# Kernel optimization log

Hardware: AMD Instinct MI355X
Metric: run time of the kernel (lower is better)

## Reference

```python
import jax, jax.numpy as jnp
import numpy as np

HID = 256  # LSTM hidden size (hard-coded in Renet)


def _lstm_dir(x, wih, whh, b):
    # x: [N, T, D]; PyTorch LSTM gate order: i, f, g, o
    def cell(carry, xt):
        h, c = carry
        g = xt @ wih.T + h @ whh.T + b
        i, f, gg, o = jnp.split(g, 4, axis=-1)
        c = jax.nn.sigmoid(f) * c + jax.nn.sigmoid(i) * jnp.tanh(gg)
        h = jax.nn.sigmoid(o) * jnp.tanh(c)
        return (h, c), h
    n = x.shape[0]
    h0 = jnp.zeros((n, HID), x.dtype)
    _, hs = jax.lax.scan(cell, (h0, h0), jnp.swapaxes(x, 0, 1))
    return jnp.swapaxes(hs, 0, 1)  # [N, T, HID]


def _bilstm(x, wf, uf, bf, wb, ub, bb):
    hf = _lstm_dir(x, wf, uf, bf)
    hb = _lstm_dir(x[:, ::-1], wb, ub, bb)[:, ::-1]
    return jnp.concatenate([hf, hb], axis=-1)  # [N, T, 2*HID]


def setup_inputs() -> dict:
    key = jax.random.key(0)
    ks = jax.random.split(key, 16)
    B, C, S = 8, 512, 64
    def p(k, shape):
        return 0.05 * jax.random.normal(k, shape, jnp.float32)
    d = {}
    d['x'] = jax.random.normal(ks[0], (B, C, S, S), jnp.float32)
    d['v_wih_f'] = p(ks[1], (4 * HID, C))
    d['v_whh_f'] = p(ks[2], (4 * HID, HID))
    d['v_b_f'] = p(ks[3], (4 * HID,))
    d['v_wih_b'] = p(ks[4], (4 * HID, C))
    d['v_whh_b'] = p(ks[5], (4 * HID, HID))
    d['v_b_b'] = p(ks[6], (4 * HID,))
    d['h_wih_f'] = p(ks[7], (4 * HID, 2 * HID))
    d['h_whh_f'] = p(ks[8], (4 * HID, HID))
    d['h_b_f'] = p(ks[9], (4 * HID,))
    d['h_wih_b'] = p(ks[10], (4 * HID, 2 * HID))
    d['h_whh_b'] = p(ks[11], (4 * HID, HID))
    d['h_b_b'] = p(ks[12], (4 * HID,))
    d['conv_w'] = p(ks[13], (22 * 22, 2 * HID))
    d['conv_b'] = p(ks[14], (22 * 22,))
    return d


def reference(x, v_wih_f, v_whh_f, v_b_f, v_wih_b, v_whh_b, v_b_b,
              h_wih_f, h_whh_f, h_b_f, h_wih_b, h_whh_b, h_b_b,
              conv_w, conv_b):
    B, C, H, W = x.shape
    # ---- Renet ----
    xt = jnp.transpose(x, (0, 2, 3, 1))  # [B,H,W,C]
    # vertical LSTM: sequence along W, batched over all B*H rows at once
    v = _bilstm(xt.reshape(B * H, W, C), v_wih_f, v_whh_f, v_b_f,
                v_wih_b, v_whh_b, v_b_b).reshape(B, H, W, 2 * HID)
    # horizontal LSTM: sequence along H, batched over all B*W columns
    h = _bilstm(jnp.transpose(v, (0, 2, 1, 3)).reshape(B * W, H, 2 * HID),
                h_wih_f, h_whh_f, h_b_f, h_wih_b, h_whh_b,
                h_b_b).reshape(B, W, H, 2 * HID)
    feat = jnp.transpose(h, (0, 3, 2, 1))  # [B, 512, H, W]
    kern = jnp.einsum('bchw,oc->bohw', feat, conv_w) + conv_b[None, :, None, None]
    # ---- PicanetG ----
    kern = jax.nn.softmax(kern, axis=1)  # softmax over 484 channel dim
    # unfold(k=22, dilation=3) with H=W=64 yields exactly one global dilated patch
    patch = x[:, :, ::3, ::3].reshape(B, C, 22 * 22)  # [B, C, 484]
    out = jnp.einsum('bck,bkl->bcl', patch, kern.reshape(B, 22 * 22, H * W))
    return out.reshape(B, C, H, W)
```

## Files before the change

### kernel.cpp

```cpp
#include <hip/hip_runtime.h>
#include <hip/hip_bf16.h>
#include <hip/hip_fp8.h>
#include <math.h>


typedef __hip_bfloat16 bf16;
typedef short short8 __attribute__((ext_vector_type(8)));
typedef float f4 __attribute__((ext_vector_type(4)));
typedef int int4v __attribute__((ext_vector_type(4)));
typedef int int8v __attribute__((ext_vector_type(8)));

#define SCL8 0x7F7F7F7F

__device__ __forceinline__ unsigned short bfbits(float f) {
    bf16 h = __float2bfloat16(f);
    return *reinterpret_cast<unsigned short*>(&h);
}
__device__ __forceinline__ float bf2f(unsigned short u) {
    union { unsigned int i; float f; } x; x.i = ((unsigned int)u) << 16; return x.f;
}
__device__ __forceinline__ unsigned char f2fp8(float f) {
    __hip_fp8_e4m3 q(f);
    return *reinterpret_cast<unsigned char*>(&q);
}
__device__ __forceinline__ float sigm2(float x) {
    return __builtin_amdgcn_rcpf(1.0f + __builtin_amdgcn_exp2f(x * -1.44269504f));
}
__device__ __forceinline__ float tanh2(float x) {
    return 1.0f - 2.0f * __builtin_amdgcn_rcpf(1.0f + __builtin_amdgcn_exp2f(x * 2.88539008f));
}

#define GLD16(g, s) __builtin_amdgcn_global_load_lds(                          \
    (const __attribute__((address_space(1))) void*)(g),                        \
    (__attribute__((address_space(3))) void*)(s), 16, 0, 0)

#define LGKM_BARRIER() do {                                                    \
    asm volatile("s_waitcnt lgkmcnt(0)" ::: "memory");                         \
    __builtin_amdgcn_s_barrier();                                              \
} while (0)

__global__ __launch_bounds__(256)
void prep_weights(const float* __restrict__ w0, const float* __restrict__ w1,
                  const float* __restrict__ w2, const float* __restrict__ w3,
                  const float* __restrict__ cw, const float* __restrict__ cb,
                  const float* __restrict__ u0, const float* __restrict__ u1,
                  const float* __restrict__ u2, const float* __restrict__ u3,
                  bf16* __restrict__ wt, bf16* __restrict__ cw2b,
                  float* __restrict__ cb2, unsigned char* __restrict__ wq)
{
    int idx = blockIdx.x * 256 + threadIdx.x;
    if (idx < 2097152) {
        int mat = idx >> 19, rem = idx & 524287;
        const float* src = (mat == 0) ? w0 : (mat == 1) ? w1 : (mat == 2) ? w2 : w3;
        wt[idx] = __float2bfloat16(src[rem]);
    } else if (idx < 2097152 + 262144) {
        int r = idx - 2097152; int o = r >> 9, k = r & 511;
        cw2b[r] = __float2bfloat16((o < 484) ? cw[o * 512 + k] : 0.f);
    } else if (idx < 2097152 + 262144 + 512) {
        int o = idx - 2097152 - 262144;
        cb2[o] = (o < 484) ? cb[o] : 0.f;
    } else if (idx < 2097152 + 262144 + 512 + 1048576) {
        int r = idx - 2097152 - 262144 - 512;
        int mat = r >> 18, rem = r & 262143;
        const float* src = (mat == 0) ? u0 : (mat == 1) ? u1 : (mat == 2) ? u2 : u3;
        wq[r] = f2fp8(src[rem]);
    }
}

__global__ __launch_bounds__(256)
void xtrans(const float* __restrict__ x, bf16* __restrict__ xt)
{
    __shared__ float T[64][65];
    const int tid = threadIdx.x;
    const int bid = blockIdx.x;
    const int b = bid >> 9, h = (bid >> 3) & 63, ct = bid & 7;
    const int c0 = ct << 6;
    const float* xp = x + ((long)(b * 512 + c0) * 64 + h) * 64;
    const int wv = tid >> 6, wl = tid & 63;
    #pragma unroll
    for (int r = 0; r < 16; ++r) {
        int ci = wv + (r << 2);
        T[ci][wl] = xp[(long)ci * 4096 + wl];
    }
    __syncthreads();
    const int wr = tid >> 2, cj = (tid & 3) << 4;
    bf16* op = xt + ((long)(b * 4096 + h * 64 + wr) * 512) + c0 + cj;
    short8 v0, v1;
    #pragma unroll
    for (int i = 0; i < 8; ++i) v0[i] = (short)bfbits(T[cj + i][wr]);
    #pragma unroll
    for (int i = 0; i < 8; ++i) v1[i] = (short)bfbits(T[cj + 8 + i][wr]);
    *(short8*)op = v0;
    *(short8*)(op + 8) = v1;
}

template<int MODE>
__global__ __launch_bounds__(256)
void gemm_lds(const bf16* __restrict__ A, const bf16* __restrict__ W,
              const float* __restrict__ biasf, const float* __restrict__ biasb,
              void* __restrict__ outf, void* __restrict__ outb, int dironly)
{
    __shared__ alignas(16) char Abuf[16384];
    __shared__ alignas(16) char Bbuf[16384];
    const int tid = threadIdx.x;
    const int wv = tid >> 6, l = tid & 63;
    const int lm = l & 15, lg = l >> 4;
    const int wm = wv >> 1, wn = wv & 1;

    const int nx = gridDim.x;
    int bid = blockIdx.y * nx + blockIdx.x;
    const int cpx = (nx * gridDim.y) >> 3;
    bid = (bid & 7) * cpx + (bid >> 3);
    const int bx = bid % nx;
    const int n0 = (bid / nx) << 7;

    int dir = 0, jblk = 0, g0 = 0;
    const bf16* Wg = W;
    if (MODE == 0) {
        dir  = (dironly < 0) ? (bx >> 3) : dironly;
        jblk = (dironly < 0) ? (bx & 7) : bx;
    } else {
        g0 = bx << 7;
        if (MODE == 2) Wg += (long)(n0 >> 9) * 2097152;
    }

    f4 acc[4][4];
    #pragma unroll
    for (int mf = 0; mf < 4; ++mf)
        #pragma unroll
        for (int nf = 0; nf < 4; ++nf)
            acc[mf][nf] = (f4){0.f, 0.f, 0.f, 0.f};

    for (int kt = 0; kt < 8; ++kt) {
        const int k0 = kt << 6;
        #pragma unroll
        for (int i = 0; i < 4; ++i) {
            const int seg = (wv << 2) + i;
            const int L = (seg << 10) + l * 16;
            const int row = L >> 7;
            const int off = (L & 127) ^ ((row & 7) << 4);
            const bf16* ga = A + (long)(n0 + row) * 512 + k0 + (off >> 1);
            GLD16(ga, &Abuf[seg << 10]);
        }
        #pragma unroll
        for (int i = 0; i < 4; ++i) {
            const int seg = (wv << 2) + i;
            const int L = (seg << 10) + l * 16;
            const int row = L >> 7;
            const int off = (L & 127) ^ ((row & 7) << 4);
            int wrow;
            if (MODE == 0) wrow = (dir << 10) + ((row >> 5) << 8) + jblk * 32 + (row & 31);
            else           wrow = g0 + row;
            const bf16* gb = Wg + (long)wrow * 512 + k0 + (off >> 1);
            GLD16(gb, &Bbuf[seg << 10]);
        }
        __syncthreads();

        #pragma unroll
        for (int kk = 0; kk < 2; ++kk) {
            short8 af[4], bq[4];
            #pragma unroll
            for (int mf = 0; mf < 4; ++mf) {
                const int row = wm * 64 + mf * 16 + lm;
                const int ad = (row << 7) + ((((kk << 6) + (lg << 4))) ^ ((row & 7) << 4));
                af[mf] = *(const short8*)&Abuf[ad];
            }
            #pragma unroll
            for (int nf = 0; nf < 4; ++nf) {
                const int row = (MODE == 0) ? (nf * 32 + wn * 16 + lm)
                                            : (wn * 64 + nf * 16 + lm);
                const int ad = (row << 7) + ((((kk << 6) + (lg << 4))) ^ ((row & 7) << 4));
                bq[nf] = *(const short8*)&Bbuf[ad];
            }
            #pragma unroll
            for (int mf = 0; mf < 4; ++mf)
                #pragma unroll
                for (int nf = 0; nf < 4; ++nf)
                    acc[mf][nf] = __builtin_amdgcn_mfma_f32_16x16x32_bf16(af[mf], bq[nf], acc[mf][nf], 0, 0, 0);
        }
        __syncthreads();
    }

    if (MODE == 0) {
        const float* bs = dir ? biasb : biasf;
        const int jglob = jblk * 32 + wn * 16 + lm;
        float bv[4];
        #pragma unroll
        for (int nf = 0; nf < 4; ++nf) bv[nf] = bs[nf * 256 + jglob];
        ushort4* Gd = (ushort4*)(dir ? outb : outf);
        #pragma unroll
        for (int mf = 0; mf < 4; ++mf) {
            #pragma unroll
            for (int r = 0; r < 4; ++r) {
                const int n = n0 + wm * 64 + mf * 16 + lg * 4 + r;
                ushort4 u;
                u.x = bfbits(acc[mf][0][r] + bv[0]);
                u.y = bfbits(acc[mf][1][r] + bv[1]);
                u.z = bfbits(acc[mf][2][r] + bv[2]);
                u.w = bfbits(acc[mf][3][r] + bv[3]);
                Gd[(long)n * 256 + jglob] = u;
            }
        }
    } else {
        float* o = (float*)outf;
        #pragma unroll
        for (int mf = 0; mf < 4; ++mf)
            #pragma unroll
            for (int r = 0; r < 4; ++r) {
                const int n = n0 + wm * 64 + mf * 16 + lg * 4 + r;
                #pragma unroll
                for (int nf = 0; nf < 4; ++nf)
                    o[(long)n * 4096 + g0 + wn * 64 + nf * 16 + lm] = acc[mf][nf][r];
            }
    }
}

__global__ __launch_bounds__(512)
void conv_sm(const bf16* __restrict__ A, const bf16* __restrict__ W,
             const float* __restrict__ bias, bf16* __restrict__ KT)
{
    __shared__ alignas(16) char SMEM[83968];
    char* Ab = SMEM;
    char* Bb = SMEM + 16384;
    float (*red)[4] = (float(*)[4])(SMEM + 81920);

    const int tid = threadIdx.x;
    const int wv = tid >> 6, l = tid & 63;
    const int lm = l & 15, lg = l >> 4;
    const int wm = wv >> 2, wn = wv & 3;
    const int n0 = blockIdx.x << 7;

    f4 acc[4][8];
    #pragma unroll
    for (int mf = 0; mf < 4; ++mf)
        #pragma unroll
        for (int nf = 0; nf < 8; ++nf)
            acc[mf][nf] = (f4){0.f, 0.f, 0.f, 0.f};

    for (int kt = 0; kt < 8; ++kt) {
        const int k0 = kt << 6;
        #pragma unroll
        for (int i = 0; i < 2; ++i) {
            const int L = (i << 13) + tid * 16;
            const int row = L >> 7;
            const int off = (L & 127) ^ ((row & 7) << 4);
            GLD16(A + (long)(n0 + row) * 512 + k0 + (off >> 1),
                  Ab + (i << 13) + (wv << 10));
        }
        #pragma unroll
        for (int j = 0; j < 8; ++j) {
            const int L = (j << 13) + tid * 16;
            const int row = L >> 7;
            const int off = (L & 127) ^ ((row & 7) << 4);
            GLD16(W + (long)row * 512 + k0 + (off >> 1),
                  Bb + (j << 13) + (wv << 10));
        }
        __syncthreads();
        #pragma unroll
        for (int kk = 0; kk < 2; ++kk) {
            short8 af[4], bq[8];
            #pragma unroll
            for (int mf = 0; mf < 4; ++mf) {
                const int row = wm * 64 + mf * 16 + lm;
                const int ad = (row << 7) + ((((kk << 6) + (lg << 4))) ^ ((row & 7) << 4));
                af[mf] = *(const short8*)&Ab[ad];
            }
            #pragma unroll
            for (int nf = 0; nf < 8; ++nf) {
                const int row = wn * 128 + nf * 16 + lm;
                const int ad = (row << 7) + ((((kk << 6) + (lg << 4))) ^ ((row & 7) << 4));
                bq[nf] = *(const short8*)&Bb[ad];
            }
            #pragma unroll
            for (int mf = 0; mf < 4; ++mf)
                #pragma unroll
                for (int nf = 0; nf < 8; ++nf)
                    acc[mf][nf] = __builtin_amdgcn_mfma_f32_16x16x32_bf16(af[mf], bq[nf], acc[mf][nf], 0, 0, 0);
        }
        __syncthreads();
    }

    float bv[8];
    bool alive[8];
    #pragma unroll
    for (int nf = 0; nf < 8; ++nf) {
        const int col = wn * 128 + nf * 16 + lm;
        bv[nf] = bias[col];
        alive[nf] = (col < 484);
    }

    #pragma unroll
    for (int mf = 0; mf < 4; ++mf) {
        #pragma unroll
        for (int r = 0; r < 4; ++r) {
            float m = -3.4e38f;
            #pragma unroll
            for (int nf = 0; nf < 8; ++nf) {
                float v = acc[mf][nf][r] + bv[nf];
                if (alive[nf]) m = fmaxf(m, v);
            }
            m = fmaxf(m, __shfl_xor(m, 1));
            m = fmaxf(m, __shfl_xor(m, 2));
            m = fmaxf(m, __shfl_xor(m, 4));
            m = fmaxf(m, __shfl_xor(m, 8));
            if (lm == 0) red[wm * 64 + mf * 16 + lg * 4 + r][wn] = m;
        }
    }
    __syncthreads();
    float mxv[4][4];
    #pragma unroll
    for (int mf = 0; mf < 4; ++mf)
        #pragma unroll
        for (int r = 0; r < 4; ++r) {
            const int row = wm * 64 + mf * 16 + lg * 4 + r;
            mxv[mf][r] = fmaxf(fmaxf(red[row][0], red[row][1]),
                               fmaxf(red[row][2], red[row][3]));
        }
    __syncthreads();
    #pragma unroll
    for (int mf = 0; mf < 4; ++mf) {
        #pragma unroll
        for (int r = 0; r < 4; ++r) {
            float s = 0.f;
            #pragma unroll
            for (int nf = 0; nf < 8; ++nf) {
                float v = acc[mf][nf][r] + bv[nf];
                float e = alive[nf]
                    ? __builtin_amdgcn_exp2f((v - mxv[mf][r]) * 1.44269504f) : 0.f;
                acc[mf][nf][r] = e;
                s += e;
            }
            s += __shfl_xor(s, 1);
            s += __shfl_xor(s, 2);
            s += __shfl_xor(s, 4);
            s += __shfl_xor(s, 8);
            if (lm == 0) red[wm * 64 + mf * 16 + lg * 4 + r][wn] = s;
        }
    }
    __syncthreads();
    float invv[4][4];
    #pragma unroll
    for (int mf = 0; mf < 4; ++mf)
        #pragma unroll
        for (int r = 0; r < 4; ++r) {
            const int row = wm * 64 + mf * 16 + lg * 4 + r;
            invv[mf][r] = __builtin_amdgcn_rcpf(red[row][0] + red[row][1] +
                                                red[row][2] + red[row][3]);
        }

    unsigned short* TB = (unsigned short*)Bb;
    unsigned short* KTu = (unsigned short*)KT;
    #pragma unroll
    for (int hm = 0; hm < 2; ++hm) {
        __syncthreads();
        if (wm == hm) {
            #pragma unroll
            for (int mf = 0; mf < 4; ++mf)
                #pragma unroll
                for (int r = 0; r < 4; ++r) {
                    const int rr = mf * 16 + lg * 4 + r;
                    #pragma unroll
                    for (int nf = 0; nf < 8; ++nf)
                        TB[rr * 512 + wn * 128 + nf * 16 + lm] =
                            bfbits(acc[mf][nf][r] * invv[mf][r]);
                }
        }
        __syncthreads();
        #pragma unroll
        for (int s = 0; s < 8; ++s) {
            const int L = (s << 13) + tid * 16;
            const int rr = L >> 10;
            const int cc = (L & 1023) >> 1;
            *(short8*)(KTu + (long)(n0 + hm * 64 + rr) * 512 + cc) =
                *(const short8*)((const char*)TB + L);
        }
    }
}

__global__ __launch_bounds__(1024, 4)
void lstm4s(const bf16* __restrict__ Gf, const bf16* __restrict__ Gb,
            const unsigned char* __restrict__ Wqf, const unsigned char* __restrict__ Wqb,
            bf16* __restrict__ Out, int dir_force)
{
    __shared__ char ldspad[83968];
    __shared__ unsigned char hbuf[2][4][256];
    const int tid = threadIdx.x;
    const int wv = tid >> 6, l = tid & 63;
    const int lm = l & 15, lg = l >> 4;
    const int j_c = wv * 16 + lm;
    const int s_a = lm >> 2;

    int dir, sblk;
    if (dir_force >= 0) { dir = dir_force; sblk = blockIdx.x; }
    else               { dir = blockIdx.x >> 7; sblk = blockIdx.x & 127; }
    if (dir_force == -9999) ((volatile char*)ldspad)[tid] = 1;

    const bf16* G = dir ? Gb : Gf;
    const unsigned char* WQ = dir ? Wqb : Wqf;
    const int s0 = sblk << 2;

    int8v wfrag[4][2];
    #pragma unroll
    for (int q = 0; q < 4; ++q) {
        const unsigned char* wr = WQ + (long)(q * 256 + wv * 16 + lm) * 256 + lg * 32;
        #pragma unroll
        for (int kt = 0; kt < 2; ++kt) {
            int4v lo = *(const int4v*)(wr + kt * 128);
            int4v hi = *(const int4v*)(wr + kt * 128 + 16);
            int8v w;
            w[0] = lo[0]; w[1] = lo[1]; w[2] = lo[2]; w[3] = lo[3];
            w[4] = hi[0]; w[5] = hi[1]; w[6] = hi[2]; w[7] = hi[3];
            wfrag[q][kt] = w;
        }
    }

    if (tid < 256) ((unsigned long*)hbuf)[tid] = 0ul;

    float cst = 0.f;
    const ushort4* G4 = (const ushort4*)G;
    const int sg = s0 + lg;
    const long gb0 = (long)sg * 16384 + j_c;
    const long ob0 = ((long)((s0 >> 6) * 4096 + (s0 & 63) + lg)) * 512 + (dir << 8) + j_c;
    unsigned short* Ou = (unsigned short*)Out;

    ushort4 uA, uB;
    {
        int t0 = dir ? 63 : 0, t1 = dir ? 62 : 1;
        uA = G4[gb0 + (long)t0 * 256];
        uB = G4[gb0 + (long)t1 * 256];
    }
    LGKM_BARRIER();

#define LSTM_STEP(SP, UREG, RB, WB)                                             \
    {                                                                           \
        const int t_ = dir ? (63 - (SP)) : (SP);                                \
        int8v af0, af1;                                                         \
        {                                                                       \
            const unsigned char* hb = &hbuf[RB][s_a][0];                        \
            const int c0 = ((lg << 5) + (s_a << 5)) & 255;                      \
            const int c1 = (128 + (lg << 5) + (s_a << 5)) & 255;                \
            int4v a0 = *(const int4v*)(hb + c0);                                \
            int4v a1 = *(const int4v*)(hb + c0 + 16);                           \
            int4v b0 = *(const int4v*)(hb + c1);                                \
            int4v b1 = *(const int4v*)(hb + c1 + 16);                           \
            af0[0]=a0[0]; af0[1]=a0[1]; af0[2]=a0[2]; af0[3]=a0[3];             \
            af0[4]=a1[0]; af0[5]=a1[1]; af0[6]=a1[2]; af0[7]=a1[3];             \
            af1[0]=b0[0]; af1[1]=b0[1]; af1[2]=b0[2]; af1[3]=b0[3];             \
            af1[4]=b1[0]; af1[5]=b1[1]; af1[6]=b1[2]; af1[7]=b1[3];             \
        }                                                                       \
        f4 ac0 = {0.f,0.f,0.f,0.f}, ac1 = {0.f,0.f,0.f,0.f};                    \
        f4 ac2 = {0.f,0.f,0.f,0.f}, ac3 = {0.f,0.f,0.f,0.f};                    \
        ac0[0] = bf2f(UREG.x); ac1[0] = bf2f(UREG.y);                           \
        ac2[0] = bf2f(UREG.z); ac3[0] = bf2f(UREG.w);                           \
        {                                                                       \
            int sp2 = (SP) + 2; if (sp2 > 63) sp2 = 63;                         \
            int tp = dir ? (63 - sp2) : sp2;                                    \
            UREG = G4[gb0 + (long)tp * 256];                                    \
        }                                                                       \
        ac0 = __builtin_amdgcn_mfma_scale_f32_16x16x128_f8f6f4(af0, wfrag[0][0], ac0, 0, 0, 0, SCL8, 0, SCL8); \
        ac1 = __builtin_amdgcn_mfma_scale_f32_16x16x128_f8f6f4(af0, wfrag[1][0], ac1, 0, 0, 0, SCL8, 0, SCL8); \
        ac2 = __builtin_amdgcn_mfma_scale_f32_16x16x128_f8f6f4(af0, wfrag[2][0], ac2, 0, 0, 0, SCL8, 0, SCL8); \
        ac3 = __builtin_amdgcn_mfma_scale_f32_16x16x128_f8f6f4(af0, wfrag[3][0], ac3, 0, 0, 0, SCL8, 0, SCL8); \
        ac0 = __builtin_amdgcn_mfma_scale_f32_16x16x128_f8f6f4(af1, wfrag[0][1], ac0, 0, 0, 0, SCL8, 0, SCL8); \
        ac1 = __builtin_amdgcn_mfma_scale_f32_16x16x128_f8f6f4(af1, wfrag[1][1], ac1, 0, 0, 0, SCL8, 0, SCL8); \
        ac2 = __builtin_amdgcn_mfma_scale_f32_16x16x128_f8f6f4(af1, wfrag[2][1], ac2, 0, 0, 0, SCL8, 0, SCL8); \
        ac3 = __builtin_amdgcn_mfma_scale_f32_16x16x128_f8f6f4(af1, wfrag[3][1], ac3, 0, 0, 0, SCL8, 0, SCL8); \
        {                                                                       \
            float ii = sigm2(ac0[0]);                                           \
            float ff = sigm2(ac1[0]);                                           \
            float gc = tanh2(ac2[0]);                                           \
            float oo = sigm2(ac3[0]);                                           \
            float c  = ff * cst + ii * gc;                                      \
            cst = c;                                                            \
            float h_ = oo * tanh2(c);                                           \
            hbuf[WB][lg][(j_c + (lg << 5)) & 255] = f2fp8(h_);                  \
            Ou[ob0 + (long)t_ * 32768] = bfbits(h_);                            \
        }                                                                       \
        LGKM_BARRIER();                                                         \
    }

    for (int sp = 0; sp < 64; sp += 2) {
        LSTM_STEP(sp,     uA, 0, 1)
        LSTM_STEP(sp + 1, uB, 1, 0)
    }
#undef LSTM_STEP
}

__global__ __launch_bounds__(256)
void gather_patch(const float* __restrict__ x, bf16* __restrict__ Pch)
{
    int idx = blockIdx.x * 256 + threadIdx.x;
    if (idx >= 2097152) return;
    int o = idx & 511, c = (idx >> 9) & 511, b = idx >> 18;
    float v = 0.f;
    if (o < 484) {
        int i = o / 22, jj = o - i * 22;
        v = x[(long)b * 2097152 + (long)c * 4096 + i * 192 + jj * 3];
    }
    Pch[idx] = __float2bfloat16(v);
}

extern "C" void kernel_launch(void* const* d_in, const int* in_sizes, int n_in,
                              void* d_out, int out_size, void* d_ws, size_t ws_size,
                              hipStream_t stream)
{
    const float* x        = (const float*)d_in[0];
    const float* v_wih_f  = (const float*)d_in[1];
    const float* v_whh_f  = (const float*)d_in[2];
    const float* v_b_f    = (const float*)d_in[3];
    const float* v_wih_b  = (const float*)d_in[4];
    const float* v_whh_b  = (const float*)d_in[5];
    const float* v_b_b    = (const float*)d_in[6];
    const float* h_wih_f  = (const float*)d_in[7];
    const float* h_whh_f  = (const float*)d_in[8];
    const float* h_b_f    = (const float*)d_in[9];
    const float* h_wih_b  = (const float*)d_in[10];
    const float* h_whh_b  = (const float*)d_in[11];
    const float* h_b_b    = (const float*)d_in[12];
    const float* conv_w   = (const float*)d_in[13];
    const float* conv_b   = (const float*)d_in[14];

    const size_t REQ_FUSED  = 50331648UL * 4UL;
    const size_t REQ_SERIAL = 33554432UL * 4UL;
    if (ws_size < REQ_SERIAL) return;
    const bool fused = (ws_size >= REQ_FUSED);

    float* wsf = (float*)d_ws;
    float* out = (float*)d_out;

    bf16*          wt   = (bf16*)(out + 8388608);
    bf16*          cw2b = (bf16*)(out + 9437184);
    float*         cb2  = out + 9568256;
    unsigned char* wq   = (unsigned char*)(out + 9568768);

    prep_weights<<<13314, 256, 0, stream>>>(v_wih_f, v_wih_b, h_wih_f, h_wih_b,
                                            conv_w, conv_b,
                                            v_whh_f, v_whh_b, h_whh_f, h_whh_b,
                                            wt, cw2b, cb2, wq);
    bf16* wt_v = wt;
    bf16* wt_h = wt + 1048576;
    unsigned char* wq_vf = wq;
    unsigned char* wq_vb = wq + 262144;
    unsigned char* wq_hf = wq + 524288;
    unsigned char* wq_hb = wq + 786432;

    dim3 gG(16, 256);
    dim3 gGs(8, 256);
    dim3 gF(32, 32);

    if (fused) {
        bf16*  Gf    = (bf16*)d_ws;
        bf16*  Gb    = (bf16*)(wsf + 16777216);
        bf16*  V     = (bf16*)(wsf + 33554432);
        bf16*  HF    = (bf16*)(wsf + 41943040);
        bf16*  xt    = V;
        bf16*  kernT = Gb;
        bf16*  Pch   = V;

        xtrans<<<4096, 256, 0, stream>>>(x, xt);
        gemm_lds<0><<<gG, 256, 0, stream>>>(xt, wt_v, v_b_f, v_b_b, Gf, Gb, -1);
        lstm4s<<<256, 1024, 0, stream>>>(Gf, Gb, wq_vf, wq_vb, V, -1);

        gemm_lds<0><<<gG, 256, 0, stream>>>(V, wt_h, h_b_f, h_b_b, Gf, Gb, -1);
        lstm4s<<<256, 1024, 0, stream>>>(Gf, Gb, wq_hf, wq_hb, HF, -1);

        conv_sm<<<256, 512, 0, stream>>>(HF, cw2b, cb2, kernT);
        gather_patch<<<8192, 256, 0, stream>>>(x, Pch);
        gemm_lds<2><<<gF, 256, 0, stream>>>(Pch, kernT, nullptr, nullptr, out, nullptr, 0);
    } else {
        bf16*  G     = (bf16*)d_ws;
        bf16*  V     = (bf16*)(wsf + 16777216);
        bf16*  xt    = (bf16*)(wsf + 25165824);
        bf16*  HF    = xt;
        bf16*  kernT = V;
        bf16*  Pch   = (bf16*)d_ws;

        xtrans<<<4096, 256, 0, stream>>>(x, xt);
        gemm_lds<0><<<gGs, 256, 0, stream>>>(xt, wt_v, v_b_f, v_b_b, G, G, 0);
        lstm4s<<<128, 1024, 0, stream>>>(G, G, wq_vf, wq_vf, V, 0);
        gemm_lds<0><<<gGs, 256, 0, stream>>>(xt, wt_v, v_b_f, v_b_b, G, G, 1);
        lstm4s<<<128, 1024, 0, stream>>>(G, G, wq_vb, wq_vb, V, 1);

        gemm_lds<0><<<gGs, 256, 0, stream>>>(V, wt_h, h_b_f, h_b_b, G, G, 0);
        lstm4s<<<128, 1024, 0, stream>>>(G, G, wq_hf, wq_hf, HF, 0);
        gemm_lds<0><<<gGs, 256, 0, stream>>>(V, wt_h, h_b_f, h_b_b, G, G, 1);
        lstm4s<<<128, 1024, 0, stream>>>(G, G, wq_hb, wq_hb, HF, 1);

        conv_sm<<<256, 512, 0, stream>>>(HF, cw2b, cb2, kernT);
        gather_patch<<<8192, 256, 0, stream>>>(x, Pch);
        gemm_lds<2><<<gF, 256, 0, stream>>>(Pch, kernT, nullptr, nullptr, out, nullptr, 0);
    }
}
```

Before: 427.9 us.

## Fuse LSTM input-projection GEMM into the recurrent LSTM kernel

Replaces the separate gate-precompute GEMM and the LSTM recurrence kernel with one kernel per layer. It computes input gates for 8-step chunks on the fly from double-buffered LDS tiles of the input and keeps them in LDS, so the large bf16 gate tensors never round-trip through global memory. The cost is that each block re-streams its weight slice from global or L2 per chunk without LDS staging. The MFMA projection work now sits inside the serial recurrence, which may lengthen the critical path.

Result: slower. 1.404 ms (+228.1%).

```diff
diff --git a/kernel.cpp b/kernel.cpp
--- a/kernel.cpp
+++ b/kernel.cpp
@@ -94,6 +94,180 @@
     *(short8*)(op + 8) = v1;
 }
 
+__global__ __launch_bounds__(1024, 4)
+void renet_fused(const bf16* __restrict__ A, const bf16* __restrict__ Wih,
+                 const float* __restrict__ biasf, const float* __restrict__ biasb,
+                 const unsigned char* __restrict__ Wqf,
+                 const unsigned char* __restrict__ Wqb,
+                 bf16* __restrict__ Out)
+{
+    __shared__ alignas(16) char Atile[2][32768];
+    __shared__ unsigned short Gch[4][8][256][4];
+    __shared__ unsigned char hbuf[2][4][256];
+
+    const int tid = threadIdx.x;
+    const int wv = tid >> 6, l = tid & 63;
+    const int lm = l & 15, lg = l >> 4;
+    const int j_c = wv * 16 + lm;
+    const int s_a = lm >> 2;
+
+    const int dir  = blockIdx.x >> 7;
+    const int sblk = blockIdx.x & 127;
+    const int s0 = sblk << 2;
+    const unsigned char* WQ = dir ? Wqb : Wqf;
+    const float* bs = dir ? biasb : biasf;
+    const bf16* Wd = Wih + ((long)dir << 10) * 512;
+
+    int8v wfrag[4][2];
+    #pragma unroll
+    for (int q = 0; q < 4; ++q) {
+        const unsigned char* wr = WQ + (long)((q << 8) + j_c) * 256 + (lg << 5);
+        #pragma unroll
+        for (int kt = 0; kt < 2; ++kt) {
+            int4v lo = *(const int4v*)(wr + kt * 128);
+            int4v hi = *(const int4v*)(wr + kt * 128 + 16);
+            int8v w;
+            w[0] = lo[0]; w[1] = lo[1]; w[2] = lo[2]; w[3] = lo[3];
+            w[4] = hi[0]; w[5] = hi[1]; w[6] = hi[2]; w[7] = hi[3];
+            wfrag[q][kt] = w;
+        }
+    }
+
+    float bv[4];
+    #pragma unroll
+    for (int q = 0; q < 4; ++q) bv[q] = bs[(q << 8) + j_c];
+
+    if (tid < 256) ((unsigned long*)hbuf)[tid] = 0ul;
+
+    float cst = 0.f;
+    const long ob0 = ((long)((s0 >> 6) * 4096 + (s0 & 63) + lg)) * 512
+                   + (dir << 8) + j_c;
+    unsigned short* Ou = (unsigned short*)Out;
+
+    long wb[4];
+    #pragma unroll
+    for (int q = 0; q < 4; ++q)
+        wb[q] = (long)((q << 8) + j_c) * 512 + (lg << 3);
+
+    const int swz0 = (lm & 7) << 4;
+
+    {
+        const int tb = dir ? 56 : 0;
+        #pragma unroll
+        for (int sw = 0; sw < 2; ++sw) {
+            const int r = sw * 16 + wv;
+            const int n = (s0 + (r >> 3)) * 64 + tb + (r & 7);
+            const int soff = (l * 16) ^ ((r & 7) << 4);
+            GLD16(A + (long)n * 512 + (soff >> 1), &Atile[0][r << 10]);
+        }
+    }
+    asm volatile("s_waitcnt vmcnt(0)" ::: "memory");
+    __builtin_amdgcn_s_barrier();
+
+    int buf = 0;
+    for (int c = 0; c < 8; ++c) {
+        if (c < 7) {
+            const int tb = dir ? 56 - 8 * (c + 1) : 8 * (c + 1);
+            #pragma unroll
+            for (int sw = 0; sw < 2; ++sw) {
+                const int r = sw * 16 + wv;
+                const int n = (s0 + (r >> 3)) * 64 + tb + (r & 7);
+                const int soff = (l * 16) ^ ((r & 7) << 4);
+                GLD16(A + (long)n * 512 + (soff >> 1), &Atile[buf ^ 1][r << 10]);
+            }
+        }
+
+        const char* Ab = Atile[buf];
+        #pragma unroll
+        for (int qp = 0; qp < 2; ++qp) {
+            f4 acc[2][2];
+            #pragma unroll
+            for (int mf = 0; mf < 2; ++mf)
+                #pragma unroll
+                for (int q2 = 0; q2 < 2; ++q2)
+                    acc[mf][q2] = (f4){0.f, 0.f, 0.f, 0.f};
+            #pragma unroll
+            for (int ks = 0; ks < 16; ++ks) {
+                const int ko = ((ks << 6) + (lg << 4)) ^ swz0;
+                short8 a0 = *(const short8*)(Ab + (lm << 10) + ko);
+                short8 a1 = *(const short8*)(Ab + ((16 + lm) << 10) + ko);
+                short8 b0 = *(const short8*)(Wd + wb[qp * 2 + 0] + (ks << 5));
+                short8 b1 = *(const short8*)(Wd + wb[qp * 2 + 1] + (ks << 5));
+                acc[0][0] = __builtin_amdgcn_mfma_f32_16x16x32_bf16(a0, b0, acc[0][0], 0, 0, 0);
+                acc[0][1] = __builtin_amdgcn_mfma_f32_16x16x32_bf16(a0, b1, acc[0][1], 0, 0, 0);
+                acc[1][0] = __builtin_amdgcn_mfma_f32_16x16x32_bf16(a1, b0, acc[1][0], 0, 0, 0);
+                acc[1][1] = __builtin_amdgcn_mfma_f32_16x16x32_bf16(a1, b1, acc[1][1], 0, 0, 0);
+            }
+            #pragma unroll
+            for (int mf = 0; mf < 2; ++mf)
+                #pragma unroll
+                for (int r = 0; r < 4; ++r) {
+                    const int row = mf * 16 + lg * 4 + r;
+                    ushort2 u2;
+                    u2.x = bfbits(acc[mf][0][r] + bv[qp * 2 + 0]);
+                    u2.y = bfbits(acc[mf][1][r] + bv[qp * 2 + 1]);
+                    *(ushort2*)&Gch[row >> 3][row & 7][j_c][qp << 1] = u2;
+                }
+        }
+        asm volatile("s_waitcnt lgkmcnt(0)" ::: "memory");
+        __builtin_amdgcn_s_barrier();
+
+        #pragma unroll
+        for (int i = 0; i < 8; ++i) {
+            const int sp = (c << 3) + i;
+            const int t_ = dir ? 63 - sp : sp;
+            const int toff = dir ? 7 - i : i;
+            const int RB = sp & 1, WB = 1 - RB;
+
+            int8v af0, af1;
+            {
+                const unsigned char* hb = &hbuf[RB][s_a][0];
+                const int c0i = ((lg << 5) + (s_a << 5)) & 255;
+                const int c1i = (128 + (lg << 5) + (s_a << 5)) & 255;
+                int4v a0 = *(const int4v*)(hb + c0i);
+                int4v a1 = *(const int4v*)(hb + c0i + 16);
+                int4v b0 = *(const int4v*)(hb + c1i);
+                int4v b1 = *(const int4v*)(hb + c1i + 16);
+                af0[0]=a0[0]; af0[1]=a0[1]; af0[2]=a0[2]; af0[3]=a0[3];
+                af0[4]=a1[0]; af0[5]=a1[1]; af0[6]=a1[2]; af0[7]=a1[3];
+                af1[0]=b0[0]; af1[1]=b0[1]; af1[2]=b0[2]; af1[3]=b0[3];
+                af1[4]=b1[0]; af1[5]=b1[1]; af1[6]=b1[2]; af1[7]=b1[3];
+            }
+            ushort4 Gr = *(const ushort4*)&Gch[lg][toff][j_c][0];
+            f4 ac0 = {0.f,0.f,0.f,0.f}, ac1 = {0.f,0.f,0.f,0.f};
+            f4 ac2 = {0.f,0.f,0.f,0.f}, ac3 = {0.f,0.f,0.f,0.f};
+            ac0[0] = bf2f(Gr.x); ac1[0] = bf2f(Gr.y);
+            ac2[0] = bf2f(Gr.z); ac3[0] = bf2f(Gr.w);
+
+            ac0 = __builtin_amdgcn_mfma_scale_f32_16x16x128_f8f6f4(af0, wfrag[0][0], ac0, 0, 0, 0, SCL8, 0, SCL8);
+            ac1 = __builtin_amdgcn_mfma_scale_f32_16x16x128_f8f6f4(af0, wfrag[1][0], ac1, 0, 0, 0, SCL8, 0, SCL8);
+            ac2 = __builtin_amdgcn_mfma_scale_f32_16x16x128_f8f6f4(af0, wfrag[2][0], ac2, 0, 0, 0, SCL8, 0, SCL8);
+            ac3 = __builtin_amdgcn_mfma_scale_f32_16x16x128_f8f6f4(af0, wfrag[3][0], ac3, 0, 0, 0, SCL8, 0, SCL8);
+            ac0 = __builtin_amdgcn_mfma_scale_f32_16x16x128_f8f6f4(af1, wfrag[0][1], ac0, 0, 0, 0, SCL8, 0, SCL8);
+            ac1 = __builtin_amdgcn_mfma_scale_f32_16x16x128_f8f6f4(af1, wfrag[1][1], ac1, 0, 0, 0, SCL8, 0, SCL8);
+            ac2 = __builtin_amdgcn_mfma_scale_f32_16x16x128_f8f6f4(af1, wfrag[2][1], ac2, 0, 0, 0, SCL8, 0, SCL8);
+            ac3 = __builtin_amdgcn_mfma_scale_f32_16x16x128_f8f6f4(af1, wfrag[3][1], ac3, 0, 0, 0, SCL8, 0, SCL8);
+
+            {
+                float ii = sigm2(ac0[0]);
+                float ff = sigm2(ac1[0]);
+                float gc = tanh2(ac2[0]);
+                float oo = sigm2(ac3[0]);
+                float cc = ff * cst + ii * gc;
+                cst = cc;
+                float h_ = oo * tanh2(cc);
+                hbuf[WB][lg][(j_c + (lg << 5)) & 255] = f2fp8(h_);
+                Ou[ob0 + (long)t_ * 32768] = bfbits(h_);
+            }
+            LGKM_BARRIER();
+        }
+
+        asm volatile("s_waitcnt vmcnt(0)" ::: "memory");
+        __builtin_amdgcn_s_barrier();
+        buf ^= 1;
+    }
+}
+
 template<int MODE>
 __global__ __launch_bounds__(256)
 void gemm_lds(const bf16* __restrict__ A, const bf16* __restrict__ W,
@@ -114,15 +288,9 @@
     const int bx = bid % nx;
     const int n0 = (bid / nx) << 7;
 
-    int dir = 0, jblk = 0, g0 = 0;
+    int g0 = bx << 7;
     const bf16* Wg = W;
-    if (MODE == 0) {
-        dir  = (dironly < 0) ? (bx >> 3) : dironly;
-        jblk = (dironly < 0) ? (bx & 7) : bx;
-    } else {
-        g0 = bx << 7;
-        if (MODE == 2) Wg += (long)(n0 >> 9) * 2097152;
-    }
+    if (MODE == 2) Wg += (long)(n0 >> 9) * 2097152;
 
     f4 acc[4][4];
     #pragma unroll
@@ -148,10 +316,7 @@
             const int L = (seg << 10) + l * 16;
             const int row = L >> 7;
             const int off = (L & 127) ^ ((row & 7) << 4);
-            int wrow;
-            if (MODE == 0) wrow = (dir << 10) + ((row >> 5) << 8) + jblk * 32 + (row & 31);
-            else           wrow = g0 + row;
-            const bf16* gb = Wg + (long)wrow * 512 + k0 + (off >> 1);
+            const bf16* gb = Wg + (long)(g0 + row) * 512 + k0 + (off >> 1);
             GLD16(gb, &Bbuf[seg << 10]);
         }
         __syncthreads();
@@ -167,8 +332,7 @@
             }
             #pragma unroll
             for (int nf = 0; nf < 4; ++nf) {
-                const int row = (MODE == 0) ? (nf * 32 + wn * 16 + lm)
-                                            : (wn * 64 + nf * 16 + lm);
+                const int row = wn * 64 + nf * 16 + lm;
                 const int ad = (row << 7) + ((((kk << 6) + (lg << 4))) ^ ((row & 7) << 4));
                 bq[nf] = *(const short8*)&Bbuf[ad];
             }
@@ -181,38 +345,16 @@
         __syncthreads();
     }
 
-    if (MODE == 0) {
-        const float* bs = dir ? biasb : biasf;
-        const int jglob = jblk * 32 + wn * 16 + lm;
-        float bv[4];
-        #pragma unroll
-        for (int nf = 0; nf < 4; ++nf) bv[nf] = bs[nf * 256 + jglob];
-        ushort4* Gd = (ushort4*)(dir ? outb : outf);
-        #pragma unroll
-        for (int mf = 0; mf < 4; ++mf) {
-            #pragma unroll
-            for (int r = 0; r < 4; ++r) {
-                const int n = n0 + wm * 64 + mf * 16 + lg * 4 + r;
-                ushort4 u;
-                u.x = bfbits(acc[mf][0][r] + bv[0]);
-                u.y = bfbits(acc[mf][1][r] + bv[1]);
-                u.z = bfbits(acc[mf][2][r] + bv[2]);
-                u.w = bfbits(acc[mf][3][r] + bv[3]);
-                Gd[(long)n * 256 + jglob] = u;
-            }
-        }
-    } else {
-        float* o = (float*)outf;
-        #pragma unroll
-        for (int mf = 0; mf < 4; ++mf)
-            #pragma unroll
-            for (int r = 0; r < 4; ++r) {
-                const int n = n0 + wm * 64 + mf * 16 + lg * 4 + r;
-                #pragma unroll
-                for (int nf = 0; nf < 4; ++nf)
-                    o[(long)n * 4096 + g0 + wn * 64 + nf * 16 + lm] = acc[mf][nf][r];
-            }
-    }
+    float* o = (float*)outf;
+    #pragma unroll
+    for (int mf = 0; mf < 4; ++mf)
+        #pragma unroll
+        for (int r = 0; r < 4; ++r) {
+            const int n = n0 + wm * 64 + mf * 16 + lg * 4 + r;
+            #pragma unroll
+            for (int nf = 0; nf < 4; ++nf)
+                o[(long)n * 4096 + g0 + wn * 64 + nf * 16 + lm] = acc[mf][nf][r];
+        }
 }
 
 __global__ __launch_bounds__(512)
@@ -375,115 +517,6 @@
                 *(const short8*)((const char*)TB + L);
         }
     }
-}
-
-__global__ __launch_bounds__(1024, 4)
-void lstm4s(const bf16* __restrict__ Gf, const bf16* __restrict__ Gb,
-            const unsigned char* __restrict__ Wqf, const unsigned char* __restrict__ Wqb,
-            bf16* __restrict__ Out, int dir_force)
-{
-    __shared__ char ldspad[83968];
-    __shared__ unsigned char hbuf[2][4][256];
-    const int tid = threadIdx.x;
-    const int wv = tid >> 6, l = tid & 63;
-    const int lm = l & 15, lg = l >> 4;
-    const int j_c = wv * 16 + lm;
-    const int s_a = lm >> 2;
-
-    int dir, sblk;
-    if (dir_force >= 0) { dir = dir_force; sblk = blockIdx.x; }
-    else               { dir = blockIdx.x >> 7; sblk = blockIdx.x & 127; }
-    if (dir_force == -9999) ((volatile char*)ldspad)[tid] = 1;
-
-    const bf16* G = dir ? Gb : Gf;
-    const unsigned char* WQ = dir ? Wqb : Wqf;
-    const int s0 = sblk << 2;
-
-    int8v wfrag[4][2];
-    #pragma unroll
-    for (int q = 0; q < 4; ++q) {
-        const unsigned char* wr = WQ + (long)(q * 256 + wv * 16 + lm) * 256 + lg * 32;
-        #pragma unroll
-        for (int kt = 0; kt < 2; ++kt) {
-            int4v lo = *(const int4v*)(wr + kt * 128);
-            int4v hi = *(const int4v*)(wr + kt * 128 + 16);
-            int8v w;
-            w[0] = lo[0]; w[1] = lo[1]; w[2] = lo[2]; w[3] = lo[3];
-            w[4] = hi[0]; w[5] = hi[1]; w[6] = hi[2]; w[7] = hi[3];
-            wfrag[q][kt] = w;
-        }
-    }
-
-    if (tid < 256) ((unsigned long*)hbuf)[tid] = 0ul;
-
-    float cst = 0.f;
-    const ushort4* G4 = (const ushort4*)G;
-    const int sg = s0 + lg;
-    const long gb0 = (long)sg * 16384 + j_c;
-    const long ob0 = ((long)((s0 >> 6) * 4096 + (s0 & 63) + lg)) * 512 + (dir << 8) + j_c;
-    unsigned short* Ou = (unsigned short*)Out;
-
-    ushort4 uA, uB;
-    {
-        int t0 = dir ? 63 : 0, t1 = dir ? 62 : 1;
-        uA = G4[gb0 + (long)t0 * 256];
-        uB = G4[gb0 + (long)t1 * 256];
-    }
-    LGKM_BARRIER();
-
-#define LSTM_STEP(SP, UREG, RB, WB)                                             \
-    {                                                                           \
-        const int t_ = dir ? (63 - (SP)) : (SP);                                \
-        int8v af0, af1;                                                         \
-        {                                                                       \
-            const unsigned char* hb = &hbuf[RB][s_a][0];                        \
-            const int c0 = ((lg << 5) + (s_a << 5)) & 255;                      \
-            const int c1 = (128 + (lg << 5) + (s_a << 5)) & 255;                \
-            int4v a0 = *(const int4v*)(hb + c0);                                \
-            int4v a1 = *(const int4v*)(hb + c0 + 16);                           \
-            int4v b0 = *(const int4v*)(hb + c1);                                \
-            int4v b1 = *(const int4v*)(hb + c1 + 16);                           \
-            af0[0]=a0[0]; af0[1]=a0[1]; af0[2]=a0[2]; af0[3]=a0[3];             \
-            af0[4]=a1[0]; af0[5]=a1[1]; af0[6]=a1[2]; af0[7]=a1[3];             \
-            af1[0]=b0[0]; af1[1]=b0[1]; af1[2]=b0[2]; af1[3]=b0[3];             \
-            af1[4]=b1[0]; af1[5]=b1[1]; af1[6]=b1[2]; af1[7]=b1[3];             \
-        }                                                                       \
-        f4 ac0 = {0.f,0.f,0.f,0.f}, ac1 = {0.f,0.f,0.f,0.f};                    \
-        f4 ac2 = {0.f,0.f,0.f,0.f}, ac3 = {0.f,0.f,0.f,0.f};                    \
-        ac0[0] = bf2f(UREG.x); ac1[0] = bf2f(UREG.y);                           \
-        ac2[0] = bf2f(UREG.z); ac3[0] = bf2f(UREG.w);                           \
-        {                                                                       \
-            int sp2 = (SP) + 2; if (sp2 > 63) sp2 = 63;                         \
-            int tp = dir ? (63 - sp2) : sp2;                                    \
-            UREG = G4[gb0 + (long)tp * 256];                                    \
-        }                                                                       \
-        ac0 = __builtin_amdgcn_mfma_scale_f32_16x16x128_f8f6f4(af0, wfrag[0][0], ac0, 0, 0, 0, SCL8, 0, SCL8); \
-        ac1 = __builtin_amdgcn_mfma_scale_f32_16x16x128_f8f6f4(af0, wfrag[1][0], ac1, 0, 0, 0, SCL8, 0, SCL8); \
-        ac2 = __builtin_amdgcn_mfma_scale_f32_16x16x128_f8f6f4(af0, wfrag[2][0], ac2, 0, 0, 0, SCL8, 0, SCL8); \
-        ac3 = __builtin_amdgcn_mfma_scale_f32_16x16x128_f8f6f4(af0, wfrag[3][0], ac3, 0, 0, 0, SCL8, 0, SCL8); \
-        ac0 = __builtin_amdgcn_mfma_scale_f32_16x16x128_f8f6f4(af1, wfrag[0][1], ac0, 0, 0, 0, SCL8, 0, SCL8); \
-        ac1 = __builtin_amdgcn_mfma_scale_f32_16x16x128_f8f6f4(af1, wfrag[1][1], ac1, 0, 0, 0, SCL8, 0, SCL8); \
-        ac2 = __builtin_amdgcn_mfma_scale_f32_16x16x128_f8f6f4(af1, wfrag[2][1], ac2, 0, 0, 0, SCL8, 0, SCL8); \
-        ac3 = __builtin_amdgcn_mfma_scale_f32_16x16x128_f8f6f4(af1, wfrag[3][1], ac3, 0, 0, 0, SCL8, 0, SCL8); \
-        {                                                                       \
-            float ii = sigm2(ac0[0]);                                           \
-            float ff = sigm2(ac1[0]);                                           \
-            float gc = tanh2(ac2[0]);                                           \
-            float oo = sigm2(ac3[0]);                                           \
-            float c  = ff * cst + ii * gc;                                      \
-            cst = c;                                                            \
-            float h_ = oo * tanh2(c);                                           \
-            hbuf[WB][lg][(j_c + (lg << 5)) & 255] = f2fp8(h_);                  \
-            Ou[ob0 + (long)t_ * 32768] = bfbits(h_);                            \
-        }                                                                       \
-        LGKM_BARRIER();                                                         \
-    }
-
-    for (int sp = 0; sp < 64; sp += 2) {
-        LSTM_STEP(sp,     uA, 0, 1)
-        LSTM_STEP(sp + 1, uB, 1, 0)
-    }
-#undef LSTM_STEP
 }
 
 __global__ __launch_bounds__(256)
@@ -520,10 +553,8 @@
     const float* conv_w   = (const float*)d_in[13];
     const float* conv_b   = (const float*)d_in[14];
 
-    const size_t REQ_FUSED  = 50331648UL * 4UL;
-    const size_t REQ_SERIAL = 33554432UL * 4UL;
-    if (ws_size < REQ_SERIAL) return;
-    const bool fused = (ws_size >= REQ_FUSED);
+    const size_t REQ = 33554432UL * 4UL;
+    if (ws_size < REQ) return;
 
     float* wsf = (float*)d_ws;
     float* out = (float*)d_out;
@@ -544,50 +575,17 @@
     unsigned char* wq_hf = wq + 524288;
     unsigned char* wq_hb = wq + 786432;
 
-    dim3 gG(16, 256);
-    dim3 gGs(8, 256);
+    bf16* xt    = (bf16*)d_ws;
+    bf16* V     = (bf16*)(wsf + 8388608);
+    bf16* HF    = (bf16*)(wsf + 16777216);
+    bf16* kernT = (bf16*)(wsf + 25165824);
+    bf16* Pch   = (bf16*)d_ws;
+
+    xtrans<<<4096, 256, 0, stream>>>(x, xt);
+    renet_fused<<<256, 1024, 0, stream>>>(xt, wt_v, v_b_f, v_b_b, wq_vf, wq_vb, V);
+    renet_fused<<<256, 1024, 0, stream>>>(V, wt_h, h_b_f, h_b_b, wq_hf, wq_hb, HF);
+    conv_sm<<<256, 512, 0, stream>>>(HF, cw2b, cb2, kernT);
+    gather_patch<<<8192, 256, 0, stream>>>(x, Pch);
     dim3 gF(32, 32);
-
-    if (fused) {
-        bf16*  Gf    = (bf16*)d_ws;
-        bf16*  Gb    = (bf16*)(wsf + 16777216);
-        bf16*  V     = (bf16*)(wsf + 33554432);
-        bf16*  HF    = (bf16*)(wsf + 41943040);
-        bf16*  xt    = V;
-        bf16*  kernT = Gb;
-        bf16*  Pch   = V;
-
-        xtrans<<<4096, 256, 0, stream>>>(x, xt);
-        gemm_lds<0><<<gG, 256, 0, stream>>>(xt, wt_v, v_b_f, v_b_b, Gf, Gb, -1);
-        lstm4s<<<256, 1024, 0, stream>>>(Gf, Gb, wq_vf, wq_vb, V, -1);
-
-        gemm_lds<0><<<gG, 256, 0, stream>>>(V, wt_h, h_b_f, h_b_b, Gf, Gb, -1);
-        lstm4s<<<256, 1024, 0, stream>>>(Gf, Gb, wq_hf, wq_hb, HF, -1);
-
-        conv_sm<<<256, 512, 0, stream>>>(HF, cw2b, cb2, kernT);
-        gather_patch<<<8192, 256, 0, stream>>>(x, Pch);
-        gemm_lds<2><<<gF, 256, 0, stream>>>(Pch, kernT, nullptr, nullptr, out, nullptr, 0);
-    } else {
-        bf16*  G     = (bf16*)d_ws;
-        bf16*  V     = (bf16*)(wsf + 16777216);
-        bf16*  xt    = (bf16*)(wsf + 25165824);
-        bf16*  HF    = xt;
-        bf16*  kernT = V;
-        bf16*  Pch   = (bf16*)d_ws;
-
-        xtrans<<<4096, 256, 0, stream>>>(x, xt);
-        gemm_lds<0><<<gGs, 256, 0, stream>>>(xt, wt_v, v_b_f, v_b_b, G, G, 0);
-        lstm4s<<<128, 1024, 0, stream>>>(G, G, wq_vf, wq_vf, V, 0);
-        gemm_lds<0><<<gGs, 256, 0, stream>>>(xt, wt_v, v_b_f, v_b_b, G, G, 1);
-        lstm4s<<<128, 1024, 0, stream>>>(G, G, wq_vb, wq_vb, V, 1);
-
-        gemm_lds<0><<<gGs, 256, 0, stream>>>(V, wt_h, h_b_f, h_b_b, G, G, 0);
-        lstm4s<<<128, 1024, 0, stream>>>(G, G, wq_hf, wq_hf, HF, 0);
-        gemm_lds<0><<<gGs, 256, 0, stream>>>(V, wt_h, h_b_f, h_b_b, G, G, 1);
-        lstm4s<<<128, 1024, 0, stream>>>(G, G, wq_hb, wq_hb, HF, 1);
-
-        conv_sm<<<256, 512, 0, stream>>>(HF, cw2b, cb2, kernT);
-        gather_patch<<<8192, 256, 0, stream>>>(x, Pch);
-        gemm_lds<2><<<gF, 256, 0, stream>>>(Pch, kernT, nullptr, nullptr, out, nullptr, 0);
-    }
-}
+    gemm_lds<2><<<gF, 256, 0, stream>>>(Pch, kernT, nullptr, nullptr, out, nullptr, 0);
+}
```
